# Performance work log

Measured on AMD Instinct MI355X. Metric: run time of the kernel, lower is better.

The kernel has to match this reference:

```python
import jax, jax.numpy as jnp
import numpy as np

M = 16
C = 7 * M          # 112, stage-8 channels
CLS = 20
TOPK = 3
NQ = 20000         # current-frame active sites at stage 8
NS = 8192          # support-frame active sites at stage 8
SCALE = 128.0      # voxel coordinate range at this depth


def setup_inputs() -> dict:
    key = jax.random.key(0)
    ks = jax.random.split(key, 9)
    coords_q = jax.random.uniform(ks[0], (NQ, 3), jnp.float32) * SCALE
    coords_s = jax.random.uniform(ks[1], (NS, 3), jnp.float32) * SCALE
    x7 = jax.random.normal(ks[2], (NQ, C), jnp.float32)
    feat_s7 = jax.random.normal(ks[3], (NS, C), jnp.float32)
    feat_s = jax.random.normal(ks[4], (NS, C), jnp.float32)
    w_attn = jax.random.normal(ks[5], (C,), jnp.float32) * 0.1
    W1 = jax.random.normal(ks[6], (2 * C, C), jnp.float32) * (1.0 / np.sqrt(2 * C))
    gamma = jnp.ones((C,), jnp.float32)
    beta = jnp.zeros((C,), jnp.float32)
    W2 = jax.random.normal(ks[7], (C, C), jnp.float32) * (1.0 / np.sqrt(C))
    W_cls = jax.random.normal(ks[8], (C, CLS), jnp.float32) * (1.0 / np.sqrt(C))
    b_cls = jnp.zeros((CLS,), jnp.float32)
    return dict(coords_q=coords_q, coords_s=coords_s, x7=x7, feat_s7=feat_s7,
                feat_s=feat_s, w_attn=w_attn, W1=W1, gamma=gamma, beta=beta,
                W2=W2, W_cls=W_cls, b_cls=b_cls)


def reference(coords_q, coords_s, x7, feat_s7, feat_s, w_attn, W1, gamma, beta, W2, W_cls, b_cls):
    # GlobalMeanAttentionPooling: attention-weighted mean over support sites -> global vector [C]
    a = jax.nn.softmax(feat_s7 @ w_attn)          # [NS]
    g = a @ feat_s7                                # [C]
    # GlobalMaskLayer: channel-wise sigmoid gating of current-frame features
    feat_q = x7 * jax.nn.sigmoid(g)                # [NQ, C]
    # DistMatchLayer_v4: top-3 nearest support voxels per query, softmax(-d2) weighting
    q2 = jnp.sum(coords_q * coords_q, -1, keepdims=True)   # [NQ, 1]
    s2 = jnp.sum(coords_s * coords_s, -1)                  # [NS]
    d2 = q2 + s2[None, :] - 2.0 * (coords_q @ coords_s.T)  # [NQ, NS]
    negd, idx = jax.lax.top_k(-d2, TOPK)                   # [NQ, K]
    w = jax.nn.softmax(negd, axis=-1)                      # [NQ, K]
    matched = jnp.einsum('nk,nkc->nc', w, feat_s[idx])     # [NQ, C]
    # tune_sub: 1x1 subconv (14m->7m) -> BN(eval affine) + ReLU -> 1x1 subconv (7m->7m)
    h = jnp.concatenate([feat_q, matched], -1) @ W1        # [NQ, C]
    h = jax.nn.relu(h * gamma + beta) @ W2                 # [NQ, C]
    # final classifier linear
    return h @ W_cls + b_cls                               # [NQ, CLS]
```

## Files before the change

### kernel.cpp

```cpp
#include <hip/hip_runtime.h>

#define NQv 20000
#define NSv 8192
#define Cv  112
#define CLSv 20
#define INFF 3.4e38f
#define JINF 0x7fffffff

#define GC 16
#define NCELL 4096
#define CELLH 8.0f
#define INVH 0.125f

#define POOLB 32
#define PT 1024
#define PNW (POOLB * PT / 64)

#define SBLK (NQv / 4)
#define MB (NQv / 32)
#define WS_START 3616
#define WS_PTS4  5668
#define WS_W1TH  38440
#define WS_W1TL  50984
#define WS_W2TH  63528
#define WS_W2TL  70696
#define WS_WCT   77864

typedef __attribute__((ext_vector_type(8))) short bf16x8;
typedef __attribute__((ext_vector_type(4))) float f32x4;
typedef unsigned short us;
typedef unsigned long long u64;

__device__ __forceinline__ float bf2f(us u) {
    union { unsigned int i; float f; } v; v.i = ((unsigned int)u) << 16; return v.f;
}
__device__ __forceinline__ us f2bf(float f) {
    union { float f; unsigned int i; } v; v.f = f;
    unsigned int r = v.i + 0x7fffu + ((v.i >> 16) & 1u);
    return (us)(r >> 16);
}
__device__ __forceinline__ void split(float v, us& h, us& l) {
    h = f2bf(v); l = f2bf(v - bf2f(h));
}

__device__ __forceinline__ u64 mkkey(float e, int j) {
    union { float f; unsigned int i; } v; v.f = e;
    unsigned int ue = v.i ^ ((unsigned int)((int)v.i >> 31) | 0x80000000u);
    return ((u64)ue << 32) | (unsigned int)j;
}
__device__ __forceinline__ float keyval(u64 k) {
    unsigned int ue = (unsigned int)(k >> 32);
    unsigned int u = ue ^ ((unsigned int)((int)(~ue) >> 31) | 0x80000000u);
    union { unsigned int i; float f; } v; v.i = u; return v.f;
}
__device__ __forceinline__ u64 umin64(u64 a, u64 b) { return a < b ? a : b; }
__device__ __forceinline__ u64 umax64(u64 a, u64 b) { return a > b ? a : b; }

__global__ __launch_bounds__(PT) void k_prep(const float* __restrict__ cs,
                                             const float* __restrict__ fs7,
                                             const float* __restrict__ wat,
                                             const float* __restrict__ W1,
                                             const float* __restrict__ W2,
                                             const float* __restrict__ Wc,
                                             float* __restrict__ ws) {
    int b = blockIdx.x, tid = threadIdx.x;

    if (b == POOLB + 1) {
        us* w1h = (us*)(ws + WS_W1TH);
        us* w1l = (us*)(ws + WS_W1TL);
        for (int idx = tid; idx < Cv * 224; idx += PT) {
            int c = idx / 224, k = idx - c * 224;
            us h, l; split(W1[k * Cv + c], h, l);
            w1h[c * 224 + k] = h; w1l[c * 224 + k] = l;
        }
        return;
    }
    if (b == POOLB + 2) {
        us* w2h = (us*)(ws + WS_W2TH);
        us* w2l = (us*)(ws + WS_W2TL);
        for (int idx = tid; idx < Cv * 128; idx += PT) {
            int c = idx >> 7, k = idx & 127;
            float v = (k < Cv) ? W2[k * Cv + c] : 0.f;
            us h, l; split(v, h, l);
            w2h[c * 128 + k] = h; w2l[c * 128 + k] = l;
        }
        float* wct = ws + WS_WCT;
        for (int idx = tid; idx < CLSv * Cv; idx += PT) {
            int cls = idx / Cv, k = idx - cls * Cv;
            wct[cls * Cv + k] = Wc[k * CLSv + cls];
        }
        return;
    }
    if (b == POOLB) {
        __shared__ int cnt[NCELL];
        __shared__ int wsum[PT / 64];
        us* startg = (us*)(ws + WS_START);
        float4* pts4 = (float4*)(ws + WS_PTS4);
        int lane = tid & 63, wv = tid >> 6;
        for (int i = tid; i < NCELL; i += PT) cnt[i] = 0;
        __syncthreads();
        float xx[8], yy[8], zz[8]; int cid[8]; int pp[8];
        #pragma unroll
        for (int k = 0; k < NSv / PT; ++k) {
            int p = k * PT + tid;
            pp[k] = p;
            xx[k] = cs[3 * p]; yy[k] = cs[3 * p + 1]; zz[k] = cs[3 * p + 2];
            int cx = (int)(xx[k] * INVH), cy = (int)(yy[k] * INVH), cz = (int)(zz[k] * INVH);
            cx = cx > 15 ? 15 : cx; cy = cy > 15 ? 15 : cy; cz = cz > 15 ? 15 : cz;
            cid[k] = (cz * GC + cy) * GC + cx;
            atomicAdd(&cnt[cid[k]], 1);
        }
        __syncthreads();
        int base = tid * 4;
        int c0 = cnt[base], c1 = cnt[base + 1], c2 = cnt[base + 2], c3 = cnt[base + 3];
        int local = c0 + c1 + c2 + c3;
        int inc = local;
        #pragma unroll
        for (int off = 1; off < 64; off <<= 1) {
            int v = __shfl_up(inc, off, 64);
            if (lane >= off) inc += v;
        }
        if (lane == 63) wsum[wv] = inc;
        __syncthreads();
        if (tid < PT / 64) {
            int v = wsum[tid];
            #pragma unroll
            for (int off = 1; off < 16; off <<= 1) {
                int o = __shfl_up(v, off, 64);
                if (tid >= off) v += o;
            }
            wsum[tid] = v;
        }
        __syncthreads();
        int wbase = (wv == 0) ? 0 : wsum[wv - 1];
        int run = wbase + inc - local;
        startg[base] = (us)run;     cnt[base] = run;     run += c0;
        startg[base + 1] = (us)run; cnt[base + 1] = run; run += c1;
        startg[base + 2] = (us)run; cnt[base + 2] = run; run += c2;
        startg[base + 3] = (us)run; cnt[base + 3] = run;
        if (tid == 0) startg[NCELL] = (us)NSv;
        __syncthreads();
        #pragma unroll
        for (int k = 0; k < NSv / PT; ++k) {
            int slot = atomicAdd(&cnt[cid[k]], 1);
            pts4[slot] = make_float4(-2.f * xx[k], -2.f * yy[k], -2.f * zz[k], (float)pp[k]);
        }
        return;
    }

    __shared__ float red[PT / 64][Cv + 1];
    int gtid = b * PT + tid;
    int wid = gtid >> 6, lw = tid >> 6, lane = gtid & 63, l2 = lane * 2;
    float2 wa = make_float2(0.f, 0.f);
    if (lane < 56) wa = *(const float2*)(wat + l2);
    float gx = 0.f, gy = 0.f, z = 0.f;
    for (int g = 0; g < 2; ++g) {
        float2 f[8]; float part[8];
        #pragma unroll
        for (int u = 0; u < 8; ++u) {
            int i = wid + (g * 8 + u) * PNW;
            f[u] = (lane < 56) ? *(const float2*)(fs7 + i * Cv + l2) : make_float2(0.f, 0.f);
            part[u] = f[u].x * wa.x + f[u].y * wa.y;
        }
        #pragma unroll
        for (int off = 32; off; off >>= 1)
            #pragma unroll
            for (int u = 0; u < 8; ++u) part[u] += __shfl_xor(part[u], off, 64);
        #pragma unroll
        for (int u = 0; u < 8; ++u) {
            float p = __expf(part[u]);
            gx = fmaf(p, f[u].x, gx); gy = fmaf(p, f[u].y, gy); z += p;
        }
    }
    if (lane < 56) { red[lw][l2] = gx; red[lw][l2 + 1] = gy; }
    if (lane == 0) red[lw][Cv] = z;
    __syncthreads();
    if (tid < Cv + 1) {
        float s = 0.f;
        #pragma unroll
        for (int i = 0; i < PT / 64; ++i) s += red[i][tid];
        ws[b * (Cv + 1) + tid] = s;
    }
}

__device__ __forceinline__ void scan_run(const float4* __restrict__ pts4,
                                         int a, int b, float qx, float qy, float qz,
                                         float& E0, float& E1, float& E2,
                                         int& J0, int& J1, int& J2) {
    for (int k = a; k < b; ++k) {
        float4 P = pts4[k];
        float x = -0.5f * P.x, y = -0.5f * P.y, z = -0.5f * P.z;
        float s2 = fmaf(x, x, fmaf(y, y, z * z));
        float e = fmaf(qx, P.x, fmaf(qy, P.y, fmaf(qz, P.z, s2)));
        int j = (int)P.w;
        bool lt2 = (e < E2) || (e == E2 && j < J2);
        if (lt2) {
            bool lt1 = (e < E1) || (e == E1 && j < J1);
            bool lt0 = (e < E0) || (e == E0 && j < J0);
            E2 = lt1 ? E1 : e;              J2 = lt1 ? J1 : j;
            E1 = lt0 ? E0 : (lt1 ? e : E1); J1 = lt0 ? J0 : (lt1 ? j : J1);
            if (lt0) { E0 = e; J0 = j; }
        }
    }
}

__global__ __launch_bounds__(256) void k_search(const float* __restrict__ cq,
                                                const float* __restrict__ ws,
                                                float* __restrict__ out) {
    const us* __restrict__ startg = (const us*)(ws + WS_START);
    const float4* __restrict__ pts4 = (const float4*)(ws + WS_PTS4);
    int tid = threadIdx.x, lane = tid & 63, widx = tid >> 6;
    int q = blockIdx.x * 4 + widx;
    float qx = cq[3 * q], qy = cq[3 * q + 1], qz = cq[3 * q + 2];
    float q2 = fmaf(qx, qx, fmaf(qy, qy, qz * qz));
    int cx = (int)(qx * INVH), cy = (int)(qy * INVH), cz = (int)(qz * INVH);
    cx = cx > 15 ? 15 : cx; cy = cy > 15 ? 15 : cy; cz = cz > 15 ? 15 : cz;
    float E0 = INFF, E1 = INFF, E2 = INFF;
    int   J0 = JINF, J1 = JINF, J2 = JINF;

    if (lane < 27) {
        int dz = lane / 9 - 1, dy = (lane / 3) % 3 - 1, dx = lane % 3 - 1;
        int xc = cx + dx, yc = cy + dy, zc = cz + dz;
        if ((unsigned)xc < 16u && (unsigned)yc < 16u && (unsigned)zc < 16u) {
            int cc = (zc * GC + yc) * GC + xc;
            scan_run(pts4, startg[cc], startg[cc + 1], qx, qy, qz, E0, E1, E2, J0, J1, J2);
        }
    }

    u64 K0, K1, K2;
    for (int s = 2; ; ++s) {
        K0 = mkkey(E0, J0); K1 = mkkey(E1, J1); K2 = mkkey(E2, J2);
        #pragma unroll
        for (int off = 1; off < 64; off <<= 1) {
            u64 b0 = __shfl_xor(K0, off, 64);
            u64 b1 = __shfl_xor(K1, off, 64);
            u64 b2 = __shfl_xor(K2, off, 64);
            u64 xx = umax64(K0, b0), yy = umin64(K1, b1);
            u64 zz = umax64(K1, b1), uu = umin64(K2, b2);
            K0 = umin64(K0, b0);
            u64 n1 = umin64(xx, yy);
            K2 = umin64(umin64(umax64(xx, yy), zz), uu);
            K1 = n1;
        }
        if (s > 15) break;

        int r = s - 1;
        int xl = cx - r > 0 ? cx - r : 0, xh = cx + r < 15 ? cx + r : 15;
        int yl = cy - r > 0 ? cy - r : 0, yh = cy + r < 15 ? cy + r : 15;
        int zl = cz - r > 0 ? cz - r : 0, zh = cz + r < 15 ? cz + r : 15;
        float fx = INFF, fy = INFF, fz = INFF;
        if (xl > 0)  fx = qx - xl * CELLH;
        if (xh < 15) fx = fminf(fx, (xh + 1) * CELLH - qx);
        if (yl > 0)  fy = qy - yl * CELLH;
        if (yh < 15) fy = fminf(fy, (yh + 1) * CELLH - qy);
        if (zl > 0)  fz = qz - zl * CELLH;
        if (zh < 15) fz = fminf(fz, (zh + 1) * CELLH - qz);
        float dmin = fminf(fx, fminf(fy, fz));
        float t2 = keyval(K2);
        if (dmin * dmin > t2 + q2 + 0.5f) break;

        int side = 2 * s + 1, s2n = side * side, tot = s2n * side;
        for (int idx = lane; idx < tot; idx += 64) {
            int dz = idx / s2n - s;
            int rem = idx - (dz + s) * s2n;
            int dy = rem / side - s;
            int dx = rem - (dy + s) * side - s;
            int ax = dx < 0 ? -dx : dx, ay = dy < 0 ? -dy : dy, az = dz < 0 ? -dz : dz;
            if (ax != s && ay != s && az != s) continue;
            int xc = cx + dx, yc = cy + dy, zc = cz + dz;
            if ((unsigned)xc > 15u || (unsigned)yc > 15u || (unsigned)zc > 15u) continue;
            int cc = (zc * GC + yc) * GC + xc;
            scan_run(pts4, startg[cc], startg[cc + 1], qx, qy, qz, E0, E1, E2, J0, J1, J2);
        }
    }
    if (lane == 0) {
        unsigned int A0 = (unsigned int)K0;
        unsigned int A1 = (unsigned int)K1;
        unsigned int A2 = (unsigned int)K2;
        if (A0 >= NSv) A0 = 0;
        if (A1 >= NSv) A1 = 0;
        if (A2 >= NSv) A2 = 0;
        ((int*)out)[q * CLSv]     = (int)(A0 | (A1 << 16));
        ((int*)out)[q * CLSv + 1] = (int)A2;
    }
}

__global__ __launch_bounds__(448) void k_mlp(
        const float* __restrict__ cq, const float* __restrict__ cs,
        const float* __restrict__ x7, const float* __restrict__ fs,
        const float* __restrict__ gma, const float* __restrict__ bta,
        const float* __restrict__ bc, const float* __restrict__ ws,
        float* __restrict__ out) {
    __shared__ __align__(16) us vbh[32 * 232];
    __shared__ __align__(16) us vbl[32 * 232];
    __shared__ __align__(16) us hbh[32 * 136];
    __shared__ __align__(16) us hbl[32 * 136];
    __shared__ __align__(16) float h2f[32 * 116];
    __shared__ float gate[Cv];
    __shared__ int   qi[32][3];
    __shared__ float qw[32][3];

    int tid = threadIdx.x;
    int q0 = blockIdx.x * 32;

    if (tid < Cv) {
        float st = 0.f, zt = 0.f;
        for (int b = 0; b < POOLB; ++b) {
            st += ws[b * (Cv + 1) + tid];
            zt += ws[b * (Cv + 1) + Cv];
        }
        gate[tid] = 1.0f / (1.0f + __expf(-(st / zt)));
    }
    int ut = tid - 128;
    if (ut >= 0 && ut < 32) {
        int q = q0 + ut;
        int A = ((const int*)out)[q * CLSv];
        int B = ((const int*)out)[q * CLSv + 1];
        int J0 = A & 0xFFFF, J1 = (A >> 16) & 0xFFFF, J2 = B;
        J0 = (J0 < 0 || J0 >= NSv) ? 0 : J0;
        J1 = (J1 < 0 || J1 >= NSv) ? 0 : J1;
        J2 = (J2 < 0 || J2 >= NSv) ? 0 : J2;
        float qx = cq[3 * q], qy = cq[3 * q + 1], qz = cq[3 * q + 2];
        float e[3]; int JJ[3] = {J0, J1, J2};
        #pragma unroll
        for (int r = 0; r < 3; ++r) {
            float x = cs[3 * JJ[r]], y = cs[3 * JJ[r] + 1], z = cs[3 * JJ[r] + 2];
            float s2 = fmaf(x, x, fmaf(y, y, z * z));
            e[r] = fmaf(qx, -2.f * x, fmaf(qy, -2.f * y, fmaf(qz, -2.f * z, s2)));
        }
        float w1v = __expf(e[0] - e[1]);
        float w2v = __expf(e[0] - e[2]);
        float iw  = 1.0f / (1.0f + w1v + w2v);
        qw[ut][0] = iw; qw[ut][1] = w1v * iw; qw[ut][2] = w2v * iw;
        qi[ut][0] = J0; qi[ut][1] = J1; qi[ut][2] = J2;
    }
    for (int i = tid; i < 32 * 16; i += 448) {
        int q = i >> 4, kk = Cv + (i & 15);
        hbh[q * 136 + kk] = 0; hbl[q * 136 + kk] = 0;
    }
    __syncthreads();

    {
        int vq = tid / 14, e = tid - vq * 14;
        int gq = q0 + vq;
        int k0 = e * 16;
        float vals[16];
        if (e < 7) {
            const float4* xr = (const float4*)(x7 + gq * Cv + k0);
            #pragma unroll
            for (int i = 0; i < 4; ++i) {
                float4 v = xr[i];
                vals[i * 4]     = v.x * gate[k0 + i * 4];
                vals[i * 4 + 1] = v.y * gate[k0 + i * 4 + 1];
                vals[i * 4 + 2] = v.z * gate[k0 + i * 4 + 2];
                vals[i * 4 + 3] = v.w * gate[k0 + i * 4 + 3];
            }
        } else {
            int kk = k0 - Cv;
            float w0 = qw[vq][0], w1v = qw[vq][1], w2v = qw[vq][2];
            const float4* r0 = (const float4*)(fs + qi[vq][0] * Cv + kk);
            const float4* r1 = (const float4*)(fs + qi[vq][1] * Cv + kk);
            const float4* r2 = (const float4*)(fs + qi[vq][2] * Cv + kk);
            #pragma unroll
            for (int i = 0; i < 4; ++i) {
                float4 a = r0[i], b = r1[i], c = r2[i];
                vals[i * 4]     = w0 * a.x + w1v * b.x + w2v * c.x;
                vals[i * 4 + 1] = w0 * a.y + w1v * b.y + w2v * c.y;
                vals[i * 4 + 2] = w0 * a.z + w1v * b.z + w2v * c.z;
                vals[i * 4 + 3] = w0 * a.w + w1v * b.w + w2v * c.w;
            }
        }
        #pragma unroll
        for (int i = 0; i < 16; ++i) {
            us h, l; split(vals[i], h, l);
            vbh[vq * 232 + k0 + i] = h;
            vbl[vq * 232 + k0 + i] = l;
        }
    }
    __syncthreads();

    int w = tid >> 6, lane = tid & 63, quad = lane >> 4, l16 = lane & 15;
    int cc = w * 16 + l16;

    {
        f32x4 acc0 = {0.f, 0.f, 0.f, 0.f};
        f32x4 acc1 = {0.f, 0.f, 0.f, 0.f};
        const us* w1h = (const us*)(ws + WS_W1TH) + cc * 224;
        const us* w1l = (const us*)(ws + WS_W1TL) + cc * 224;
        #pragma unroll
        for (int ks = 0; ks < 7; ++ks) {
            int ko = ks * 32 + quad * 8;
            bf16x8 bh  = *(const bf16x8*)(w1h + ko);
            bf16x8 bl  = *(const bf16x8*)(w1l + ko);
            bf16x8 a0h = *(const bf16x8*)(vbh + l16 * 232 + ko);
            bf16x8 a0l = *(const bf16x8*)(vbl + l16 * 232 + ko);
            bf16x8 a1h = *(const bf16x8*)(vbh + (l16 + 16) * 232 + ko);
            bf16x8 a1l = *(const bf16x8*)(vbl + (l16 + 16) * 232 + ko);
            acc0 = __builtin_amdgcn_mfma_f32_16x16x32_bf16(a0h, bh, acc0, 0, 0, 0);
            acc0 = __builtin_amdgcn_mfma_f32_16x16x32_bf16(a0l, bh, acc0, 0, 0, 0);
            acc0 = __builtin_amdgcn_mfma_f32_16x16x32_bf16(a0h, bl, acc0, 0, 0, 0);
            acc1 = __builtin_amdgcn_mfma_f32_16x16x32_bf16(a1h, bh, acc1, 0, 0, 0);
            acc1 = __builtin_amdgcn_mfma_f32_16x16x32_bf16(a1l, bh, acc1, 0, 0, 0);
            acc1 = __builtin_amdgcn_mfma_f32_16x16x32_bf16(a1h, bl, acc1, 0, 0, 0);
        }
        float g = gma[cc], bb = bta[cc];
        #pragma unroll
        for (int r = 0; r < 4; ++r) {
            int q = quad * 4 + r;
            float h = fmaf(acc0[r], g, bb); h = h > 0.f ? h : 0.f;
            us hh, ll; split(h, hh, ll);
            hbh[q * 136 + cc] = hh; hbl[q * 136 + cc] = ll;
            float h2 = fmaf(acc1[r], g, bb); h2 = h2 > 0.f ? h2 : 0.f;
            split(h2, hh, ll);
            hbh[(q + 16) * 136 + cc] = hh; hbl[(q + 16) * 136 + cc] = ll;
        }
    }
    __syncthreads();

    {
        f32x4 acc0 = {0.f, 0.f, 0.f, 0.f};
        f32x4 acc1 = {0.f, 0.f, 0.f, 0.f};
        const us* w2h = (const us*)(ws + WS_W2TH) + cc * 128;
        const us* w2l = (const us*)(ws + WS_W2TL) + cc * 128;
        #pragma unroll
        for (int ks = 0; ks < 4; ++ks) {
            int ko = ks * 32 + quad * 8;
            bf16x8 bh  = *(const bf16x8*)(w2h + ko);
            bf16x8 bl  = *(const bf16x8*)(w2l + ko);
            bf16x8 a0h = *(const bf16x8*)(hbh + l16 * 136 + ko);
            bf16x8 a0l = *(const bf16x8*)(hbl + l16 * 136 + ko);
            bf16x8 a1h = *(const bf16x8*)(hbh + (l16 + 16) * 136 + ko);
            bf16x8 a1l = *(const bf16x8*)(hbl + (l16 + 16) * 136 + ko);
            acc0 = __builtin_amdgcn_mfma_f32_16x16x32_bf16(a0h, bh, acc0, 0, 0, 0);
            acc0 = __builtin_amdgcn_mfma_f32_16x16x32_bf16(a0l, bh, acc0, 0, 0, 0);
            acc0 = __builtin_amdgcn_mfma_f32_16x16x32_bf16(a0h, bl, acc0, 0, 0, 0);
            acc1 = __builtin_amdgcn_mfma_f32_16x16x32_bf16(a1h, bh, acc1, 0, 0, 0);
            acc1 = __builtin_amdgcn_mfma_f32_16x16x32_bf16(a1l, bh, acc1, 0, 0, 0);
            acc1 = __builtin_amdgcn_mfma_f32_16x16x32_bf16(a1h, bl, acc1, 0, 0, 0);
        }
        #pragma unroll
        for (int r = 0; r < 4; ++r) {
            int q = quad * 4 + r;
            h2f[q * 116 + cc] = acc0[r];
            h2f[(q + 16) * 116 + cc] = acc1[r];
        }
    }
    __syncthreads();

    for (int it = tid; it < 32 * CLSv; it += 448) {
        int cls = it % CLSv, qq = it / CLSv;
        const float4* wr = (const float4*)(ws + WS_WCT + cls * Cv);
        const float4* hr = (const float4*)(h2f + qq * 116);
        float a = bc[cls];
        #pragma unroll 7
        for (int i = 0; i < 28; ++i) {
            float4 h = hr[i], v = wr[i];
            a = fmaf(h.x, v.x, fmaf(h.y, v.y, fmaf(h.z, v.z, fmaf(h.w, v.w, a))));
        }
        out[(q0 + qq) * CLSv + cls] = a;
    }
}

extern "C" void kernel_launch(void* const* d_in, const int* in_sizes, int n_in,
                              void* d_out, int out_size, void* d_ws, size_t ws_size,
                              hipStream_t stream) {
    const float* cq  = (const float*)d_in[0];
    const float* cs  = (const float*)d_in[1];
    const float* x7  = (const float*)d_in[2];
    const float* fs7 = (const float*)d_in[3];
    const float* fs  = (const float*)d_in[4];
    const float* wat = (const float*)d_in[5];
    const float* W1  = (const float*)d_in[6];
    const float* gma = (const float*)d_in[7];
    const float* bta = (const float*)d_in[8];
    const float* W2  = (const float*)d_in[9];
    const float* Wc  = (const float*)d_in[10];
    const float* bc  = (const float*)d_in[11];
    float* ws  = (float*)d_ws;
    float* out = (float*)d_out;

    k_prep<<<POOLB + 3, PT, 0, stream>>>(cs, fs7, wat, W1, W2, Wc, ws);
    k_search<<<SBLK, 256, 0, stream>>>(cq, ws, out);
    k_mlp<<<MB, 448, 0, stream>>>(cq, cs, x7, fs, gma, bta, bc, ws, out);
}
```

Measured before the change: 154.6 us.

## Fuse grid kNN search into MLP kernel with 16 lanes per query

Removes the separate k_search kernel and performs the neighbor search inside the MLP kernel, with 16 lanes per query (32 queries per 512-thread block) instead of a full 64-lane wave per query. Softmax weights now come from the search keys directly, so support coordinates are no longer re-read and the index round-trip through the output buffer goes away. This cuts one launch and a global handoff, and makes better use of lanes that were mostly idle in the 64-wide search. In exchange, each query has fewer lanes for large shells, and wave-level divergence between queries that finish the search at different radii serialises work before the MLP phase.

```diff
diff --git a/kernel.cpp b/kernel.cpp
--- a/kernel.cpp
+++ b/kernel.cpp
@@ -16,8 +16,8 @@
 #define PT 1024
 #define PNW (POOLB * PT / 64)
 
-#define SBLK (NQv / 4)
 #define MB (NQv / 32)
+#define MT 512
 #define WS_START 3616
 #define WS_PTS4  5668
 #define WS_W1TH  38440
@@ -204,89 +204,8 @@
     }
 }
 
-__global__ __launch_bounds__(256) void k_search(const float* __restrict__ cq,
-                                                const float* __restrict__ ws,
-                                                float* __restrict__ out) {
-    const us* __restrict__ startg = (const us*)(ws + WS_START);
-    const float4* __restrict__ pts4 = (const float4*)(ws + WS_PTS4);
-    int tid = threadIdx.x, lane = tid & 63, widx = tid >> 6;
-    int q = blockIdx.x * 4 + widx;
-    float qx = cq[3 * q], qy = cq[3 * q + 1], qz = cq[3 * q + 2];
-    float q2 = fmaf(qx, qx, fmaf(qy, qy, qz * qz));
-    int cx = (int)(qx * INVH), cy = (int)(qy * INVH), cz = (int)(qz * INVH);
-    cx = cx > 15 ? 15 : cx; cy = cy > 15 ? 15 : cy; cz = cz > 15 ? 15 : cz;
-    float E0 = INFF, E1 = INFF, E2 = INFF;
-    int   J0 = JINF, J1 = JINF, J2 = JINF;
-
-    if (lane < 27) {
-        int dz = lane / 9 - 1, dy = (lane / 3) % 3 - 1, dx = lane % 3 - 1;
-        int xc = cx + dx, yc = cy + dy, zc = cz + dz;
-        if ((unsigned)xc < 16u && (unsigned)yc < 16u && (unsigned)zc < 16u) {
-            int cc = (zc * GC + yc) * GC + xc;
-            scan_run(pts4, startg[cc], startg[cc + 1], qx, qy, qz, E0, E1, E2, J0, J1, J2);
-        }
-    }
-
-    u64 K0, K1, K2;
-    for (int s = 2; ; ++s) {
-        K0 = mkkey(E0, J0); K1 = mkkey(E1, J1); K2 = mkkey(E2, J2);
-        #pragma unroll
-        for (int off = 1; off < 64; off <<= 1) {
-            u64 b0 = __shfl_xor(K0, off, 64);
-            u64 b1 = __shfl_xor(K1, off, 64);
-            u64 b2 = __shfl_xor(K2, off, 64);
-            u64 xx = umax64(K0, b0), yy = umin64(K1, b1);
-            u64 zz = umax64(K1, b1), uu = umin64(K2, b2);
-            K0 = umin64(K0, b0);
-            u64 n1 = umin64(xx, yy);
-            K2 = umin64(umin64(umax64(xx, yy), zz), uu);
-            K1 = n1;
-        }
-        if (s > 15) break;
-
-        int r = s - 1;
-        int xl = cx - r > 0 ? cx - r : 0, xh = cx + r < 15 ? cx + r : 15;
-        int yl = cy - r > 0 ? cy - r : 0, yh = cy + r < 15 ? cy + r : 15;
-        int zl = cz - r > 0 ? cz - r : 0, zh = cz + r < 15 ? cz + r : 15;
-        float fx = INFF, fy = INFF, fz = INFF;
-        if (xl > 0)  fx = qx - xl * CELLH;
-        if (xh < 15) fx = fminf(fx, (xh + 1) * CELLH - qx);
-        if (yl > 0)  fy = qy - yl * CELLH;
-        if (yh < 15) fy = fminf(fy, (yh + 1) * CELLH - qy);
-        if (zl > 0)  fz = qz - zl * CELLH;
-        if (zh < 15) fz = fminf(fz, (zh + 1) * CELLH - qz);
-        float dmin = fminf(fx, fminf(fy, fz));
-        float t2 = keyval(K2);
-        if (dmin * dmin > t2 + q2 + 0.5f) break;
-
-        int side = 2 * s + 1, s2n = side * side, tot = s2n * side;
-        for (int idx = lane; idx < tot; idx += 64) {
-            int dz = idx / s2n - s;
-            int rem = idx - (dz + s) * s2n;
-            int dy = rem / side - s;
-            int dx = rem - (dy + s) * side - s;
-            int ax = dx < 0 ? -dx : dx, ay = dy < 0 ? -dy : dy, az = dz < 0 ? -dz : dz;
-            if (ax != s && ay != s && az != s) continue;
-            int xc = cx + dx, yc = cy + dy, zc = cz + dz;
-            if ((unsigned)xc > 15u || (unsigned)yc > 15u || (unsigned)zc > 15u) continue;
-            int cc = (zc * GC + yc) * GC + xc;
-            scan_run(pts4, startg[cc], startg[cc + 1], qx, qy, qz, E0, E1, E2, J0, J1, J2);
-        }
-    }
-    if (lane == 0) {
-        unsigned int A0 = (unsigned int)K0;
-        unsigned int A1 = (unsigned int)K1;
-        unsigned int A2 = (unsigned int)K2;
-        if (A0 >= NSv) A0 = 0;
-        if (A1 >= NSv) A1 = 0;
-        if (A2 >= NSv) A2 = 0;
-        ((int*)out)[q * CLSv]     = (int)(A0 | (A1 << 16));
-        ((int*)out)[q * CLSv + 1] = (int)A2;
-    }
-}
-
-__global__ __launch_bounds__(448) void k_mlp(
-        const float* __restrict__ cq, const float* __restrict__ cs,
+__global__ __launch_bounds__(MT) void k_fused(
+        const float* __restrict__ cq,
         const float* __restrict__ x7, const float* __restrict__ fs,
         const float* __restrict__ gma, const float* __restrict__ bta,
         const float* __restrict__ bc, const float* __restrict__ ws,
@@ -300,6 +219,9 @@
     __shared__ int   qi[32][3];
     __shared__ float qw[32][3];
 
+    const us* __restrict__ startg = (const us*)(ws + WS_START);
+    const float4* __restrict__ pts4 = (const float4*)(ws + WS_PTS4);
+
     int tid = threadIdx.x;
     int q0 = blockIdx.x * 32;
 
@@ -311,36 +233,106 @@
         }
         gate[tid] = 1.0f / (1.0f + __expf(-(st / zt)));
     }
-    int ut = tid - 128;
-    if (ut >= 0 && ut < 32) {
-        int q = q0 + ut;
-        int A = ((const int*)out)[q * CLSv];
-        int B = ((const int*)out)[q * CLSv + 1];
-        int J0 = A & 0xFFFF, J1 = (A >> 16) & 0xFFFF, J2 = B;
-        J0 = (J0 < 0 || J0 >= NSv) ? 0 : J0;
-        J1 = (J1 < 0 || J1 >= NSv) ? 0 : J1;
-        J2 = (J2 < 0 || J2 >= NSv) ? 0 : J2;
+    {
+        int q = tid >> 4, kk = Cv + (tid & 15);
+        hbh[q * 136 + kk] = 0; hbl[q * 136 + kk] = 0;
+    }
+
+    {
+        int sub = tid & 15;
+        int qq  = tid >> 4;
+        int q   = q0 + qq;
         float qx = cq[3 * q], qy = cq[3 * q + 1], qz = cq[3 * q + 2];
-        float e[3]; int JJ[3] = {J0, J1, J2};
-        #pragma unroll
-        for (int r = 0; r < 3; ++r) {
-            float x = cs[3 * JJ[r]], y = cs[3 * JJ[r] + 1], z = cs[3 * JJ[r] + 2];
-            float s2 = fmaf(x, x, fmaf(y, y, z * z));
-            e[r] = fmaf(qx, -2.f * x, fmaf(qy, -2.f * y, fmaf(qz, -2.f * z, s2)));
-        }
-        float w1v = __expf(e[0] - e[1]);
-        float w2v = __expf(e[0] - e[2]);
-        float iw  = 1.0f / (1.0f + w1v + w2v);
-        qw[ut][0] = iw; qw[ut][1] = w1v * iw; qw[ut][2] = w2v * iw;
-        qi[ut][0] = J0; qi[ut][1] = J1; qi[ut][2] = J2;
-    }
-    for (int i = tid; i < 32 * 16; i += 448) {
-        int q = i >> 4, kk = Cv + (i & 15);
-        hbh[q * 136 + kk] = 0; hbl[q * 136 + kk] = 0;
+        float q2 = fmaf(qx, qx, fmaf(qy, qy, qz * qz));
+        int cx = (int)(qx * INVH), cy = (int)(qy * INVH), cz = (int)(qz * INVH);
+        cx = cx > 15 ? 15 : cx; cy = cy > 15 ? 15 : cy; cz = cz > 15 ? 15 : cz;
+        float E0 = INFF, E1 = INFF, E2 = INFF;
+        int   J0 = JINF, J1 = JINF, J2 = JINF;
+
+        #pragma unroll
+        for (int c = sub; c < 27; c += 16) {
+            int dz = c / 9 - 1, dy = (c / 3) % 3 - 1, dx = c % 3 - 1;
+            int xc = cx + dx, yc = cy + dy, zc = cz + dz;
+            if ((unsigned)xc < 16u && (unsigned)yc < 16u && (unsigned)zc < 16u) {
+                int ccell = (zc * GC + yc) * GC + xc;
+                scan_run(pts4, startg[ccell], startg[ccell + 1], qx, qy, qz,
+                         E0, E1, E2, J0, J1, J2);
+            }
+        }
+
+        u64 K0 = ~0ull, K1 = ~0ull, K2 = ~0ull;
+        bool done = false;
+        for (int s = 2; ; ++s) {
+            if (!done) {
+                K0 = mkkey(E0, J0); K1 = mkkey(E1, J1); K2 = mkkey(E2, J2);
+                #pragma unroll
+                for (int off = 1; off < 16; off <<= 1) {
+                    u64 b0 = __shfl_xor(K0, off, 64);
+                    u64 b1 = __shfl_xor(K1, off, 64);
+                    u64 b2 = __shfl_xor(K2, off, 64);
+                    u64 xx = umax64(K0, b0), yy = umin64(K1, b1);
+                    u64 zz = umax64(K1, b1), uu = umin64(K2, b2);
+                    K0 = umin64(K0, b0);
+                    u64 n1 = umin64(xx, yy);
+                    K2 = umin64(umin64(umax64(xx, yy), zz), uu);
+                    K1 = n1;
+                }
+            }
+            if (s > 15) break;
+            if (!done) {
+                int r = s - 1;
+                int xl = cx - r > 0 ? cx - r : 0, xh = cx + r < 15 ? cx + r : 15;
+                int yl = cy - r > 0 ? cy - r : 0, yh = cy + r < 15 ? cy + r : 15;
+                int zl = cz - r > 0 ? cz - r : 0, zh = cz + r < 15 ? cz + r : 15;
+                float fx = INFF, fy = INFF, fz = INFF;
+                if (xl > 0)  fx = qx - xl * CELLH;
+                if (xh < 15) fx = fminf(fx, (xh + 1) * CELLH - qx);
+                if (yl > 0)  fy = qy - yl * CELLH;
+                if (yh < 15) fy = fminf(fy, (yh + 1) * CELLH - qy);
+                if (zl > 0)  fz = qz - zl * CELLH;
+                if (zh < 15) fz = fminf(fz, (zh + 1) * CELLH - qz);
+                float dmin = fminf(fx, fminf(fy, fz));
+                float t2 = keyval(K2);
+                if (dmin * dmin > t2 + q2 + 0.5f) {
+                    done = true;
+                } else {
+                    int side = 2 * s + 1, s2n = side * side, tot = s2n * side;
+                    for (int idx = sub; idx < tot; idx += 16) {
+                        int dz = idx / s2n - s;
+                        int rem = idx - (dz + s) * s2n;
+                        int dy = rem / side - s;
+                        int dx = rem - (dy + s) * side - s;
+                        int ax = dx < 0 ? -dx : dx, ay = dy < 0 ? -dy : dy, az = dz < 0 ? -dz : dz;
+                        if (ax != s && ay != s && az != s) continue;
+                        int xc = cx + dx, yc = cy + dy, zc = cz + dz;
+                        if ((unsigned)xc > 15u || (unsigned)yc > 15u || (unsigned)zc > 15u) continue;
+                        int ccell = (zc * GC + yc) * GC + xc;
+                        scan_run(pts4, startg[ccell], startg[ccell + 1], qx, qy, qz,
+                                 E0, E1, E2, J0, J1, J2);
+                    }
+                }
+            }
+            if (__all(done)) break;
+        }
+
+        if (sub == 0) {
+            unsigned int A0 = (unsigned int)K0;
+            unsigned int A1 = (unsigned int)K1;
+            unsigned int A2 = (unsigned int)K2;
+            if (A0 >= NSv) A0 = 0;
+            if (A1 >= NSv) A1 = 0;
+            if (A2 >= NSv) A2 = 0;
+            float e0 = keyval(K0), e1 = keyval(K1), e2 = keyval(K2);
+            float w1v = __expf(e0 - e1);
+            float w2v = __expf(e0 - e2);
+            float iw  = 1.0f / (1.0f + w1v + w2v);
+            qw[qq][0] = iw; qw[qq][1] = w1v * iw; qw[qq][2] = w2v * iw;
+            qi[qq][0] = (int)A0; qi[qq][1] = (int)A1; qi[qq][2] = (int)A2;
+        }
     }
     __syncthreads();
 
-    {
+    if (tid < 448) {
         int vq = tid / 14, e = tid - vq * 14;
         int gq = q0 + vq;
         int k0 = e * 16;
@@ -382,7 +374,7 @@
     int w = tid >> 6, lane = tid & 63, quad = lane >> 4, l16 = lane & 15;
     int cc = w * 16 + l16;
 
-    {
+    if (w < 7) {
         f32x4 acc0 = {0.f, 0.f, 0.f, 0.f};
         f32x4 acc1 = {0.f, 0.f, 0.f, 0.f};
         const us* w1h = (const us*)(ws + WS_W1TH) + cc * 224;
@@ -417,7 +409,7 @@
     }
     __syncthreads();
 
-    {
+    if (w < 7) {
         f32x4 acc0 = {0.f, 0.f, 0.f, 0.f};
         f32x4 acc1 = {0.f, 0.f, 0.f, 0.f};
         const us* w2h = (const us*)(ws + WS_W2TH) + cc * 128;
@@ -447,7 +439,7 @@
     }
     __syncthreads();
 
-    for (int it = tid; it < 32 * CLSv; it += 448) {
+    for (int it = tid; it < 32 * CLSv; it += MT) {
         int cls = it % CLSv, qq = it / CLSv;
         const float4* wr = (const float4*)(ws + WS_WCT + cls * Cv);
         const float4* hr = (const float4*)(h2f + qq * 116);
@@ -480,6 +472,5 @@
     float* out = (float*)d_out;
 
     k_prep<<<POOLB + 3, PT, 0, stream>>>(cs, fs7, wat, W1, W2, Wc, ws);
-    k_search<<<SBLK, 256, 0, stream>>>(cq, ws, out);
-    k_mlp<<<MB, 448, 0, stream>>>(cq, cs, x7, fs, gma, bta, bc, ws, out);
-}
+    k_fused<<<MB, MT, 0, stream>>>(cq, x7, fs, gma, bta, bc, ws, out);
+}
```

After: 153.4 us. Within noise of the previous version (-0.8%).
